# Kernel optimization log

Measured on AMD Instinct MI355X. Metric: run time of the kernel, lower is better.

## Reference

```python
import jax, jax.numpy as jnp
import numpy as np

N = 100000   # nodes
E = 1600000  # edges (avg degree 16)
D = 128      # input_dim = hidden_dim = output_dim


def setup_inputs() -> dict:
    key = jax.random.key(0)
    ks = jax.random.split(key, 16)
    s = 0.02
    inp = {
        "node_emb": jax.random.normal(ks[0], (N, D), dtype=jnp.float32),
        "edge_index": jax.random.randint(ks[1], (2, E), 0, N, dtype=jnp.int64),
        # last-layer GCN branch (conv1 -> relu -> conv2); earlier layers are dead code in SSL.forward
        "gcn_w1": jax.random.normal(ks[2], (D, D), dtype=jnp.float32) * s,
        "gcn_b1": jnp.zeros((D,), dtype=jnp.float32),
        "gcn_w2": jax.random.normal(ks[3], (D, D), dtype=jnp.float32) * s,
        "gcn_b2": jnp.zeros((D,), dtype=jnp.float32),
        # last-layer GIN branch (GINConv eps=0, Mlp == single Linear)
        "gin_w1": jax.random.normal(ks[4], (D, D), dtype=jnp.float32) * s,
        "gin_b1": jnp.zeros((D,), dtype=jnp.float32),
        "gin_w2": jax.random.normal(ks[5], (D, D), dtype=jnp.float32) * s,
        "gin_b2": jnp.zeros((D,), dtype=jnp.float32),
        # fusion heads
        "lin_w": jax.random.normal(ks[6], (D, D), dtype=jnp.float32) * s,
        "lin_b": jnp.zeros((D,), dtype=jnp.float32),
        "fc_w": jax.random.normal(ks[7], (D, D), dtype=jnp.float32) * s,
        "fc_b": jnp.zeros((D,), dtype=jnp.float32),
    }
    return inp


def reference(node_emb, edge_index, gcn_w1, gcn_b1, gcn_w2, gcn_b2,
              gin_w1, gin_b1, gin_w2, gin_b2, lin_w, lin_b, fc_w, fc_b):
    n = node_emb.shape[0]
    src, dst = edge_index[0], edge_index[1]

    # symmetric GCN normalization with self-loops: deg counts incoming edges + 1
    deg = jax.ops.segment_sum(jnp.ones(src.shape[0], node_emb.dtype), dst, num_segments=n) + 1.0
    dinv = jax.lax.rsqrt(deg)                  # deg >= 1 always
    edge_norm = dinv[src] * dinv[dst]          # [E]
    self_norm = dinv * dinv                    # [N] self-loop coefficient

    def gcn_conv(x, W, b):
        y = x @ W                                                        # [N, D]
        agg = jax.ops.segment_sum(y[src] * edge_norm[:, None], dst, num_segments=n)
        return agg + self_norm[:, None] * y + b

    def gin_conv(x, W, b):
        # GINConv(train_eps=False): nn((1+0)*x + sum_{j in N(i)} x_j), nn = Linear
        agg = jax.ops.segment_sum(x[src], dst, num_segments=n)
        return (x + agg) @ W + b

    # GCN branch: conv1 -> relu -> (dropout=identity in eval) -> conv2
    h = jax.nn.relu(gcn_conv(node_emb, gcn_w1, gcn_b1))
    x_gcn = gcn_conv(h, gcn_w2, gcn_b2)

    # GIN branch: conv1 -> conv2
    g = gin_conv(node_emb, gin_w1, gin_b1)
    x_gin = gin_conv(g, gin_w2, gin_b2)

    # fusion heads
    x_gin = x_gin @ lin_w + lin_b
    x_gcn = x_gcn @ lin_w + lin_b
    return (x_gin + x_gcn) @ fc_w + fc_b
```

## Files before the change

kernel.cpp:

```cpp
#include <hip/hip_runtime.h>

#define D 128
#define HS_LD 136

using s8v = __attribute__((ext_vector_type(8))) short;
using f4v = __attribute__((ext_vector_type(4))) float;

__device__ __forceinline__ float bf2f(ushort u) {
  union { uint i; float f; } v; v.i = ((uint)u) << 16; return v.f;
}
__device__ __forceinline__ ushort f2bf(float f) {
  union { float f; uint i; } v; v.f = f;
  uint b = v.i;
  return (ushort)((b + 0x7fffu + ((b >> 16) & 1u)) >> 16);
}

__global__ void megaA_kernel(const int* __restrict__ dst, int* __restrict__ ideg,
                             int* __restrict__ pos, int E,
                             const float* __restrict__ x, ushort* __restrict__ xb, long total,
                             const float* __restrict__ lw, const float* __restrict__ fw,
                             float* __restrict__ LF,
                             const float* __restrict__ gw1, ushort* __restrict__ T1g) {
  int b = blockIdx.x;
  if (b < 2048) {
    int i = b * 256 + threadIdx.x;
    int stride = 2048 * 256;
    for (int e = i; e < E; e += stride)
      pos[e] = atomicAdd(&ideg[dst[e]], 1);
  } else if (b < 5248) {
    long i = ((long)(b - 2048) * 256 + threadIdx.x) * 8;
    long stride = (long)3200 * 256 * 8;
    for (long t = i; t < total; t += stride) {
      float4 v0 = *(const float4*)(x + t);
      float4 v1 = *(const float4*)(x + t + 4);
      s8v u;
      u[0] = (short)f2bf(v0.x); u[1] = (short)f2bf(v0.y);
      u[2] = (short)f2bf(v0.z); u[3] = (short)f2bf(v0.w);
      u[4] = (short)f2bf(v1.x); u[5] = (short)f2bf(v1.y);
      u[6] = (short)f2bf(v1.z); u[7] = (short)f2bf(v1.w);
      *(s8v*)(xb + t) = u;
    }
  } else if (b < 5312) {
    int t = (b - 5248) * 256 + threadIdx.x;
    int r = t >> 7, c = t & 127;
    float s = 0.f;
#pragma unroll 8
    for (int k = 0; k < 128; ++k) s = fmaf(lw[r * 128 + k], fw[k * 128 + c], s);
    LF[r * 128 + c] = s;
  } else {
    int t = (b - 5312) * 256 + threadIdx.x;
    int k = t >> 7, c = t & 127;
    T1g[c * 128 + k] = f2bf(gw1[k * 128 + c]);
  }
}

__global__ void scanP_kernel(const int* __restrict__ deg, int* __restrict__ incl,
                             int* __restrict__ bsum, int n, int nb,
                             const float* __restrict__ iw2, const float* __restrict__ gw2,
                             const float* __restrict__ LF,
                             float* __restrict__ M2i, ushort* __restrict__ W2gT,
                             const float* __restrict__ gb2, const float* __restrict__ ib2,
                             const float* __restrict__ lb, const float* __restrict__ fw,
                             const float* __restrict__ fb, float* __restrict__ btot) {
  int b = blockIdx.x;
  if (b < nb) {
    __shared__ int tmp[256];
    int t = threadIdx.x;
    int i = b * 256 + t;
    int v = (i < n) ? deg[i] : 0;
    tmp[t] = v;
    __syncthreads();
#pragma unroll
    for (int off = 1; off < 256; off <<= 1) {
      int u = (t >= off) ? tmp[t - off] : 0;
      __syncthreads();
      tmp[t] += u;
      __syncthreads();
    }
    if (i < n) incl[i] = tmp[t];
    if (t == 255) bsum[b] = tmp[255];
  } else if (b < nb + 64) {
    int t = (b - nb) * 256 + threadIdx.x;
    int k = t >> 7, c = t & 127;
    float s = 0.f;
#pragma unroll 8
    for (int j = 0; j < 128; ++j) s = fmaf(iw2[k * 128 + j], LF[j * 128 + c], s);
    M2i[k * 128 + c] = s;
  } else if (b < nb + 128) {
    int t = (b - nb - 64) * 256 + threadIdx.x;
    int k = t >> 7, c = t & 127;
    float s = 0.f;
#pragma unroll 8
    for (int j = 0; j < 128; ++j) s = fmaf(gw2[k * 128 + j], LF[j * 128 + c], s);
    W2gT[c * 128 + k] = f2bf(s);
  } else if (threadIdx.x < 128) {
    int c = threadIdx.x;
    float s = fb[c];
#pragma unroll 8
    for (int j = 0; j < 128; ++j) {
      s = fmaf(gb2[j] + ib2[j], LF[j * 128 + c], s);
      s = fmaf(2.f * lb[j], fw[j * 128 + c], s);
    }
    btot[c] = s;
  }
}

__global__ void scan2F_kernel(int* __restrict__ bsum, int nb,
                              const float* __restrict__ iw1, const float* __restrict__ M2i,
                              ushort* __restrict__ WginT,
                              const float* __restrict__ ib1, float* __restrict__ bgin) {
  int b = blockIdx.x;
  if (b == 0) {
    __shared__ int tmp[256];
    __shared__ int carry_s;
    int t = threadIdx.x;
    if (t == 0) carry_s = 0;
    __syncthreads();
    for (int base = 0; base < nb; base += 256) {
      int v = (base + t < nb) ? bsum[base + t] : 0;
      tmp[t] = v;
      __syncthreads();
#pragma unroll
      for (int off = 1; off < 256; off <<= 1) {
        int u = (t >= off) ? tmp[t - off] : 0;
        __syncthreads();
        tmp[t] += u;
        __syncthreads();
      }
      int inc = tmp[t] + carry_s;
      if (base + t < nb) bsum[base + t] = inc;
      __syncthreads();
      if (t == 255) carry_s = inc;
      __syncthreads();
    }
  } else if (b <= 64) {
    int t = (b - 1) * 256 + threadIdx.x;
    int k = t >> 7, c = t & 127;
    float s = 0.f;
#pragma unroll 8
    for (int j = 0; j < 128; ++j) s = fmaf(iw1[k * 128 + j], M2i[j * 128 + c], s);
    WginT[c * 128 + k] = f2bf(s);
  } else if (threadIdx.x < 128) {
    int c = threadIdx.x;
    float s = 0.f;
#pragma unroll 8
    for (int j = 0; j < 128; ++j) s = fmaf(ib1[j], M2i[j * 128 + c], s);
    bgin[c] = s;
  }
}

__global__ void scan3_kernel(const int* __restrict__ deg, const int* __restrict__ incl,
                             const int* __restrict__ bsum, int* __restrict__ rowptr,
                             float* __restrict__ dinv, int n, int E) {
  int i = blockIdx.x * 256 + threadIdx.x;
  if (i < n) {
    int carry = (blockIdx.x > 0) ? bsum[blockIdx.x - 1] : 0;
    int d = deg[i];
    rowptr[i] = incl[i] - d + carry;
    dinv[i] = rsqrtf((float)d + 1.0f);
  }
  if (i == 0) rowptr[n] = E;
}

__global__ void scatter_kernel(const int* __restrict__ src, const int* __restrict__ dst,
                               const int* __restrict__ rowptr, const int* __restrict__ pos,
                               int* __restrict__ csrc, int E) {
  int i = blockIdx.x * blockDim.x + threadIdx.x;
  int stride = gridDim.x * blockDim.x;
  for (int e = i; e < E; e += stride)
    csrc[rowptr[dst[e]] + pos[e]] = src[e];
}

__global__ __launch_bounds__(256) void gatherA_kernel(
    const ushort* __restrict__ xb, const float* __restrict__ dinv,
    const int* __restrict__ rowptr, const int* __restrict__ csrc,
    ushort* __restrict__ ab, int n) {
  int nd = blockIdx.x * 4 + (threadIdx.x >> 6);
  if (nd >= n) return;
  int lane = threadIdx.x & 63;
  int half = lane >> 5;
  int hl = lane & 31;
  int beg = rowptr[nd], end = rowptr[nd + 1];
  float4 sg = make_float4(0.f, 0.f, 0.f, 0.f);
  float4 sc = make_float4(0.f, 0.f, 0.f, 0.f);
  int j = beg + half;
  for (; j + 6 < end; j += 8) {
    int s0 = csrc[j], s1 = csrc[j + 2], s2 = csrc[j + 4], s3 = csrc[j + 6];
    float w0 = dinv[s0], w1 = dinv[s1], w2 = dinv[s2], w3 = dinv[s3];
    ushort4 v0 = *(const ushort4*)(xb + (long)s0 * D + 4 * hl);
    ushort4 v1 = *(const ushort4*)(xb + (long)s1 * D + 4 * hl);
    ushort4 v2 = *(const ushort4*)(xb + (long)s2 * D + 4 * hl);
    ushort4 v3 = *(const ushort4*)(xb + (long)s3 * D + 4 * hl);
    float a0 = bf2f(v0.x), a1 = bf2f(v0.y), a2 = bf2f(v0.z), a3 = bf2f(v0.w);
    sg.x += a0; sg.y += a1; sg.z += a2; sg.w += a3;
    sc.x = fmaf(w0, a0, sc.x); sc.y = fmaf(w0, a1, sc.y);
    sc.z = fmaf(w0, a2, sc.z); sc.w = fmaf(w0, a3, sc.w);
    a0 = bf2f(v1.x); a1 = bf2f(v1.y); a2 = bf2f(v1.z); a3 = bf2f(v1.w);
    sg.x += a0; sg.y += a1; sg.z += a2; sg.w += a3;
    sc.x = fmaf(w1, a0, sc.x); sc.y = fmaf(w1, a1, sc.y);
    sc.z = fmaf(w1, a2, sc.z); sc.w = fmaf(w1, a3, sc.w);
    a0 = bf2f(v2.x); a1 = bf2f(v2.y); a2 = bf2f(v2.z); a3 = bf2f(v2.w);
    sg.x += a0; sg.y += a1; sg.z += a2; sg.w += a3;
    sc.x = fmaf(w2, a0, sc.x); sc.y = fmaf(w2, a1, sc.y);
    sc.z = fmaf(w2, a2, sc.z); sc.w = fmaf(w2, a3, sc.w);
    a0 = bf2f(v3.x); a1 = bf2f(v3.y); a2 = bf2f(v3.z); a3 = bf2f(v3.w);
    sg.x += a0; sg.y += a1; sg.z += a2; sg.w += a3;
    sc.x = fmaf(w3, a0, sc.x); sc.y = fmaf(w3, a1, sc.y);
    sc.z = fmaf(w3, a2, sc.z); sc.w = fmaf(w3, a3, sc.w);
  }
  for (; j < end; j += 2) {
    int s0 = csrc[j];
    float w0 = dinv[s0];
    ushort4 v0 = *(const ushort4*)(xb + (long)s0 * D + 4 * hl);
    float a0 = bf2f(v0.x), a1 = bf2f(v0.y), a2 = bf2f(v0.z), a3 = bf2f(v0.w);
    sg.x += a0; sg.y += a1; sg.z += a2; sg.w += a3;
    sc.x = fmaf(w0, a0, sc.x); sc.y = fmaf(w0, a1, sc.y);
    sc.z = fmaf(w0, a2, sc.z); sc.w = fmaf(w0, a3, sc.w);
  }
  sg.x += __shfl_xor(sg.x, 32); sg.y += __shfl_xor(sg.y, 32);
  sg.z += __shfl_xor(sg.z, 32); sg.w += __shfl_xor(sg.w, 32);
  sc.x += __shfl_xor(sc.x, 32); sc.y += __shfl_xor(sc.y, 32);
  sc.z += __shfl_xor(sc.z, 32); sc.w += __shfl_xor(sc.w, 32);

  ushort4 us = *(const ushort4*)(xb + (long)nd * D + 4 * hl);
  float x0 = bf2f(us.x), x1 = bf2f(us.y), x2 = bf2f(us.z), x3 = bf2f(us.w);
  float dd = dinv[nd];
  ushort4 o;
  if (half == 0) {
    o.x = f2bf(dd * (sc.x + dd * x0));
    o.y = f2bf(dd * (sc.y + dd * x1));
    o.z = f2bf(dd * (sc.z + dd * x2));
    o.w = f2bf(dd * (sc.w + dd * x3));
    *(ushort4*)(ab + (long)nd * 256 + 4 * hl) = o;
  } else {
    o.x = f2bf(x0 + sg.x);
    o.y = f2bf(x1 + sg.y);
    o.z = f2bf(x2 + sg.z);
    o.w = f2bf(x3 + sg.w);
    *(ushort4*)(ab + (long)nd * 256 + 128 + 4 * hl) = o;
  }
}

__global__ __launch_bounds__(256) void gemm1_kernel(
    const ushort* __restrict__ ab,
    const ushort* __restrict__ T1g, const ushort* __restrict__ WginT,
    const ushort* __restrict__ W2gT,
    const float* __restrict__ gb1, const float* __restrict__ bgin,
    ushort* __restrict__ pq, int n) {
  __shared__ ushort Ws[128 * 128];
  __shared__ ushort Hs[128 * HS_LD];
  const int y = blockIdx.y;
  const int tid = threadIdx.x;
  const int wave = tid >> 6, lane = tid & 63;
  const int rlo = lane & 15, khi = lane >> 4;
  const int rb = blockIdx.x * 128 + wave * 32;

  s8v a[2][4];
#pragma unroll
  for (int rt = 0; rt < 2; ++rt) {
    int row = rb + rt * 16 + rlo;
    row = row < n ? row : n - 1;
    const ushort* p = ab + (long)row * 256 + y * 128 + khi * 8;
#pragma unroll
    for (int ks = 0; ks < 4; ++ks) a[rt][ks] = *(const s8v*)(p + ks * 32);
  }

  {
    const ushort* W = y ? WginT : T1g;
#pragma unroll
    for (int j = 0; j < 8; ++j) {
      int q = tid + 256 * j;
      int c = q >> 4, kc = q & 15;
      *(s8v*)&Ws[c * 128 + ((kc ^ (c & 7)) << 3)] = *(const s8v*)(W + c * 128 + kc * 8);
    }
  }
  __syncthreads();

  f4v acc[2][8];
#pragma unroll
  for (int rt = 0; rt < 2; ++rt)
#pragma unroll
    for (int ct = 0; ct < 8; ++ct) acc[rt][ct] = (f4v){0.f, 0.f, 0.f, 0.f};

#pragma unroll
  for (int ks = 0; ks < 4; ++ks) {
#pragma unroll
    for (int ct = 0; ct < 8; ++ct) {
      int c = ct * 16 + rlo;
      int kc = ks * 4 + khi;
      s8v b = *(const s8v*)&Ws[c * 128 + ((kc ^ (c & 7)) << 3)];
      acc[0][ct] = __builtin_amdgcn_mfma_f32_16x16x32_bf16(a[0][ks], b, acc[0][ct], 0, 0, 0);
      acc[1][ct] = __builtin_amdgcn_mfma_f32_16x16x32_bf16(a[1][ks], b, acc[1][ct], 0, 0, 0);
    }
  }

  if (y == 1) {
#pragma unroll
    for (int ct = 0; ct < 8; ++ct) {
      int col = ct * 16 + rlo;
      float bb = bgin[col];
#pragma unroll
      for (int rt = 0; rt < 2; ++rt) {
#pragma unroll
        for (int i = 0; i < 4; ++i) {
          int row = rb + rt * 16 + 4 * khi + i;
          if (row < n)
            pq[(long)row * 256 + 128 + col] = f2bf(acc[rt][ct][i] + bb);
        }
      }
    }
    return;
  }

  __syncthreads();
#pragma unroll
  for (int ct = 0; ct < 8; ++ct) {
    int col = ct * 16 + rlo;
    float bb = gb1[col];
#pragma unroll
    for (int rt = 0; rt < 2; ++rt) {
#pragma unroll
      for (int i = 0; i < 4; ++i) {
        int r = wave * 32 + rt * 16 + 4 * khi + i;
        Hs[r * HS_LD + col] = f2bf(fmaxf(acc[rt][ct][i] + bb, 0.f));
      }
    }
  }
#pragma unroll
  for (int j = 0; j < 8; ++j) {
    int q = tid + 256 * j;
    int c = q >> 4, kc = q & 15;
    *(s8v*)&Ws[c * 128 + ((kc ^ (c & 7)) << 3)] = *(const s8v*)(W2gT + c * 128 + kc * 8);
  }
  __syncthreads();

  s8v a2[2][4];
#pragma unroll
  for (int rt = 0; rt < 2; ++rt) {
    int r = wave * 32 + rt * 16 + rlo;
#pragma unroll
    for (int ks = 0; ks < 4; ++ks)
      a2[rt][ks] = *(const s8v*)&Hs[r * HS_LD + (ks * 4 + khi) * 8];
  }

  f4v acc2[2][8];
#pragma unroll
  for (int rt = 0; rt < 2; ++rt)
#pragma unroll
    for (int ct = 0; ct < 8; ++ct) acc2[rt][ct] = (f4v){0.f, 0.f, 0.f, 0.f};

#pragma unroll
  for (int ks = 0; ks < 4; ++ks) {
#pragma unroll
    for (int ct = 0; ct < 8; ++ct) {
      int c = ct * 16 + rlo;
      int kc = ks * 4 + khi;
      s8v b = *(const s8v*)&Ws[c * 128 + ((kc ^ (c & 7)) << 3)];
      acc2[0][ct] = __builtin_amdgcn_mfma_f32_16x16x32_bf16(a2[0][ks], b, acc2[0][ct], 0, 0, 0);
      acc2[1][ct] = __builtin_amdgcn_mfma_f32_16x16x32_bf16(a2[1][ks], b, acc2[1][ct], 0, 0, 0);
    }
  }

#pragma unroll
  for (int ct = 0; ct < 8; ++ct) {
    int col = ct * 16 + rlo;
#pragma unroll
    for (int rt = 0; rt < 2; ++rt) {
#pragma unroll
      for (int i = 0; i < 4; ++i) {
        int row = rb + rt * 16 + 4 * khi + i;
        if (row < n)
          pq[(long)row * 256 + col] = f2bf(acc2[rt][ct][i]);
      }
    }
  }
}

__global__ __launch_bounds__(256) void gatherB_kernel(
    const ushort* __restrict__ pq, const float* __restrict__ dinv,
    const int* __restrict__ rowptr, const int* __restrict__ csrc,
    const float* __restrict__ btot, float* __restrict__ out, int n) {
  int nd = blockIdx.x * 4 + (threadIdx.x >> 6);
  if (nd >= n) return;
  int lane = threadIdx.x & 63;
  int half = lane >> 5;
  int hl = lane & 31;
  int beg = rowptr[nd], end = rowptr[nd + 1];
  float4 s = make_float4(0.f, 0.f, 0.f, 0.f);
  int j = beg;
  for (; j + 3 < end; j += 4) {
    int s0 = csrc[j], s1 = csrc[j + 1], s2 = csrc[j + 2], s3 = csrc[j + 3];
    float w0 = dinv[s0], w1 = dinv[s1], w2 = dinv[s2], w3 = dinv[s3];
    ushort4 v0 = *(const ushort4*)(pq + (long)s0 * 256 + lane * 4);
    ushort4 v1 = *(const ushort4*)(pq + (long)s1 * 256 + lane * 4);
    ushort4 v2 = *(const ushort4*)(pq + (long)s2 * 256 + lane * 4);
    ushort4 v3 = *(const ushort4*)(pq + (long)s3 * 256 + lane * 4);
    float c0 = half ? 1.f : w0;
    float c1 = half ? 1.f : w1;
    float c2 = half ? 1.f : w2;
    float c3 = half ? 1.f : w3;
    s.x = fmaf(c0, bf2f(v0.x), s.x); s.y = fmaf(c0, bf2f(v0.y), s.y);
    s.z = fmaf(c0, bf2f(v0.z), s.z); s.w = fmaf(c0, bf2f(v0.w), s.w);
    s.x = fmaf(c1, bf2f(v1.x), s.x); s.y = fmaf(c1, bf2f(v1.y), s.y);
    s.z = fmaf(c1, bf2f(v1.z), s.z); s.w = fmaf(c1, bf2f(v1.w), s.w);
    s.x = fmaf(c2, bf2f(v2.x), s.x); s.y = fmaf(c2, bf2f(v2.y), s.y);
    s.z = fmaf(c2, bf2f(v2.z), s.z); s.w = fmaf(c2, bf2f(v2.w), s.w);
    s.x = fmaf(c3, bf2f(v3.x), s.x); s.y = fmaf(c3, bf2f(v3.y), s.y);
    s.z = fmaf(c3, bf2f(v3.z), s.z); s.w = fmaf(c3, bf2f(v3.w), s.w);
  }
  for (; j < end; ++j) {
    int s0 = csrc[j];
    float w0 = dinv[s0];
    ushort4 v0 = *(const ushort4*)(pq + (long)s0 * 256 + lane * 4);
    float c0 = half ? 1.f : w0;
    s.x = fmaf(c0, bf2f(v0.x), s.x); s.y = fmaf(c0, bf2f(v0.y), s.y);
    s.z = fmaf(c0, bf2f(v0.z), s.z); s.w = fmaf(c0, bf2f(v0.w), s.w);
  }
  ushort4 u = *(const ushort4*)(pq + (long)nd * 256 + lane * 4);
  float dd = dinv[nd];
  float4 o;
  if (half == 0) {
    o.x = dd * (s.x + dd * bf2f(u.x));
    o.y = dd * (s.y + dd * bf2f(u.y));
    o.z = dd * (s.z + dd * bf2f(u.z));
    o.w = dd * (s.w + dd * bf2f(u.w));
  } else {
    o.x = s.x + bf2f(u.x);
    o.y = s.y + bf2f(u.y);
    o.z = s.z + bf2f(u.z);
    o.w = s.w + bf2f(u.w);
  }
  o.x += __shfl_xor(o.x, 32);
  o.y += __shfl_xor(o.y, 32);
  o.z += __shfl_xor(o.z, 32);
  o.w += __shfl_xor(o.w, 32);
  if (half == 0) {
    float4 bt = *(const float4*)(btot + 4 * hl);
    o.x += bt.x; o.y += bt.y; o.z += bt.z; o.w += bt.w;
    *(float4*)(out + (long)nd * D + 4 * hl) = o;
  }
}

extern "C" void kernel_launch(void* const* d_in, const int* in_sizes, int n_in,
                              void* d_out, int out_size, void* d_ws, size_t ws_size,
                              hipStream_t stream) {
  const float* x   = (const float*)d_in[0];
  const int*   ei  = (const int*)d_in[1];
  const float* gw1 = (const float*)d_in[2];
  const float* gb1 = (const float*)d_in[3];
  const float* gw2 = (const float*)d_in[4];
  const float* gb2 = (const float*)d_in[5];
  const float* iw1 = (const float*)d_in[6];
  const float* ib1 = (const float*)d_in[7];
  const float* iw2 = (const float*)d_in[8];
  const float* ib2 = (const float*)d_in[9];
  const float* lw  = (const float*)d_in[10];
  const float* lb  = (const float*)d_in[11];
  const float* fw  = (const float*)d_in[12];
  const float* fb  = (const float*)d_in[13];
  float* out = (float*)d_out;

  const int n = in_sizes[0] / D;
  const int E = in_sizes[1] / 2;
  const int* src = ei;
  const int* dst = ei + E;
  const int nb = (n + 255) / 256;
  const long ND = (long)n * D;

  char* p = (char*)d_ws;
  auto alloc = [&](size_t bytes) {
    char* r = p;
    p += (bytes + 255) & ~(size_t)255;
    return r;
  };
  int* ideg    = (int*)alloc((size_t)n * 4);
  int* incl    = (int*)alloc((size_t)n * 4);
  int* rowptr  = (int*)alloc((size_t)(n + 1) * 4);
  int* bsum    = (int*)alloc(1024 * 4);
  int* pos     = (int*)alloc((size_t)E * 4);
  int* csrc    = (int*)alloc((size_t)E * 4);
  float* dinv  = (float*)alloc((size_t)n * 4);
  float* LF    = (float*)alloc(16384 * 4);
  float* M2i   = (float*)alloc(16384 * 4);
  float* btot  = (float*)alloc(128 * 4);
  float* bgin  = (float*)alloc(128 * 4);
  ushort* xb   = (ushort*)alloc(ND * 2);
  ushort* T1g   = (ushort*)alloc(16384 * 2);
  ushort* WginT = (ushort*)alloc(16384 * 2);
  ushort* W2gT  = (ushort*)alloc(16384 * 2);
  ushort* ab   = (ushort*)alloc(2 * ND * 2);
  ushort* pq   = (ushort*)alloc(2 * ND * 2);

  hipMemsetAsync(ideg, 0, (size_t)n * 4, stream);

  megaA_kernel<<<5376, 256, 0, stream>>>(dst, ideg, pos, E, x, xb, ND, lw, fw, LF, gw1, T1g);
  scanP_kernel<<<nb + 129, 256, 0, stream>>>(ideg, incl, bsum, n, nb, iw2, gw2, LF,
                                             M2i, W2gT, gb2, ib2, lb, fw, fb, btot);
  scan2F_kernel<<<66, 256, 0, stream>>>(bsum, nb, iw1, M2i, WginT, ib1, bgin);
  scan3_kernel<<<nb, 256, 0, stream>>>(ideg, incl, bsum, rowptr, dinv, n, E);
  scatter_kernel<<<2048, 256, 0, stream>>>(src, dst, rowptr, pos, csrc, E);

  gatherA_kernel<<<(n + 3) / 4, 256, 0, stream>>>(xb, dinv, rowptr, csrc, ab, n);
  const int nblk = (n + 127) / 128;
  gemm1_kernel<<<dim3(nblk, 2), 256, 0, stream>>>(ab, T1g, WginT, W2gT, gb1, bgin, pq, n);
  gatherB_kernel<<<(n + 3) / 4, 256, 0, stream>>>(pq, dinv, rowptr, csrc, btot, out, n);
}
```

Before: 374.3 us.

## Pack source index with dinv in CSR and prescale GCN rows by dinv

The scatter kernel now writes an int2 per CSR edge holding the source id and that source's dinv. gatherA reads the weight from this contiguous array instead of doing a random dinv lookup per edge. gemm1 multiplies its output rows by dinv before writing pq, so gatherB sums neighbour rows without any per-edge weight and drops its dinv gathers and FMAs. In exchange, the CSR array doubles in size and the scatter kernel does one extra random dinv read per edge. Correctness depends on the prescale being applied only to the GCN half of pq.

```diff
diff --git a/kernel.cpp b/kernel.cpp
--- a/kernel.cpp
+++ b/kernel.cpp
@@ -164,16 +164,19 @@
 
 __global__ void scatter_kernel(const int* __restrict__ src, const int* __restrict__ dst,
                                const int* __restrict__ rowptr, const int* __restrict__ pos,
-                               int* __restrict__ csrc, int E) {
+                               const float* __restrict__ dinv,
+                               int2* __restrict__ cdata, int E) {
   int i = blockIdx.x * blockDim.x + threadIdx.x;
   int stride = gridDim.x * blockDim.x;
-  for (int e = i; e < E; e += stride)
-    csrc[rowptr[dst[e]] + pos[e]] = src[e];
+  for (int e = i; e < E; e += stride) {
+    int s = src[e];
+    cdata[rowptr[dst[e]] + pos[e]] = make_int2(s, __float_as_int(dinv[s]));
+  }
 }
 
 __global__ __launch_bounds__(256) void gatherA_kernel(
     const ushort* __restrict__ xb, const float* __restrict__ dinv,
-    const int* __restrict__ rowptr, const int* __restrict__ csrc,
+    const int* __restrict__ rowptr, const int2* __restrict__ cd,
     ushort* __restrict__ ab, int n) {
   int nd = blockIdx.x * 4 + (threadIdx.x >> 6);
   if (nd >= n) return;
@@ -185,12 +188,13 @@
   float4 sc = make_float4(0.f, 0.f, 0.f, 0.f);
   int j = beg + half;
   for (; j + 6 < end; j += 8) {
-    int s0 = csrc[j], s1 = csrc[j + 2], s2 = csrc[j + 4], s3 = csrc[j + 6];
-    float w0 = dinv[s0], w1 = dinv[s1], w2 = dinv[s2], w3 = dinv[s3];
-    ushort4 v0 = *(const ushort4*)(xb + (long)s0 * D + 4 * hl);
-    ushort4 v1 = *(const ushort4*)(xb + (long)s1 * D + 4 * hl);
-    ushort4 v2 = *(const ushort4*)(xb + (long)s2 * D + 4 * hl);
-    ushort4 v3 = *(const ushort4*)(xb + (long)s3 * D + 4 * hl);
+    int2 c0 = cd[j], c1 = cd[j + 2], c2 = cd[j + 4], c3 = cd[j + 6];
+    float w0 = __int_as_float(c0.y), w1 = __int_as_float(c1.y);
+    float w2 = __int_as_float(c2.y), w3 = __int_as_float(c3.y);
+    ushort4 v0 = *(const ushort4*)(xb + (long)c0.x * D + 4 * hl);
+    ushort4 v1 = *(const ushort4*)(xb + (long)c1.x * D + 4 * hl);
+    ushort4 v2 = *(const ushort4*)(xb + (long)c2.x * D + 4 * hl);
+    ushort4 v3 = *(const ushort4*)(xb + (long)c3.x * D + 4 * hl);
     float a0 = bf2f(v0.x), a1 = bf2f(v0.y), a2 = bf2f(v0.z), a3 = bf2f(v0.w);
     sg.x += a0; sg.y += a1; sg.z += a2; sg.w += a3;
     sc.x = fmaf(w0, a0, sc.x); sc.y = fmaf(w0, a1, sc.y);
@@ -209,9 +213,9 @@
     sc.z = fmaf(w3, a2, sc.z); sc.w = fmaf(w3, a3, sc.w);
   }
   for (; j < end; j += 2) {
-    int s0 = csrc[j];
-    float w0 = dinv[s0];
-    ushort4 v0 = *(const ushort4*)(xb + (long)s0 * D + 4 * hl);
+    int2 c0 = cd[j];
+    float w0 = __int_as_float(c0.y);
+    ushort4 v0 = *(const ushort4*)(xb + (long)c0.x * D + 4 * hl);
     float a0 = bf2f(v0.x), a1 = bf2f(v0.y), a2 = bf2f(v0.z), a3 = bf2f(v0.w);
     sg.x += a0; sg.y += a1; sg.z += a2; sg.w += a3;
     sc.x = fmaf(w0, a0, sc.x); sc.y = fmaf(w0, a1, sc.y);
@@ -246,6 +250,7 @@
     const ushort* __restrict__ T1g, const ushort* __restrict__ WginT,
     const ushort* __restrict__ W2gT,
     const float* __restrict__ gb1, const float* __restrict__ bgin,
+    const float* __restrict__ dinv,
     ushort* __restrict__ pq, int n) {
   __shared__ ushort Ws[128 * 128];
   __shared__ ushort Hs[128 * HS_LD];
@@ -361,6 +366,15 @@
     }
   }
 
+  float ddv[2][4];
+#pragma unroll
+  for (int rt = 0; rt < 2; ++rt)
+#pragma unroll
+    for (int i = 0; i < 4; ++i) {
+      int row = rb + rt * 16 + 4 * khi + i;
+      ddv[rt][i] = (row < n) ? dinv[row] : 0.f;
+    }
+
 #pragma unroll
   for (int ct = 0; ct < 8; ++ct) {
     int col = ct * 16 + rlo;
@@ -370,7 +384,7 @@
       for (int i = 0; i < 4; ++i) {
         int row = rb + rt * 16 + 4 * khi + i;
         if (row < n)
-          pq[(long)row * 256 + col] = f2bf(acc2[rt][ct][i]);
+          pq[(long)row * 256 + col] = f2bf(ddv[rt][i] * acc2[rt][ct][i]);
       }
     }
   }
@@ -378,7 +392,7 @@
 
 __global__ __launch_bounds__(256) void gatherB_kernel(
     const ushort* __restrict__ pq, const float* __restrict__ dinv,
-    const int* __restrict__ rowptr, const int* __restrict__ csrc,
+    const int* __restrict__ rowptr, const int2* __restrict__ cd,
     const float* __restrict__ btot, float* __restrict__ out, int n) {
   int nd = blockIdx.x * 4 + (threadIdx.x >> 6);
   if (nd >= n) return;
@@ -389,41 +403,30 @@
   float4 s = make_float4(0.f, 0.f, 0.f, 0.f);
   int j = beg;
   for (; j + 3 < end; j += 4) {
-    int s0 = csrc[j], s1 = csrc[j + 1], s2 = csrc[j + 2], s3 = csrc[j + 3];
-    float w0 = dinv[s0], w1 = dinv[s1], w2 = dinv[s2], w3 = dinv[s3];
+    int s0 = cd[j].x, s1 = cd[j + 1].x, s2 = cd[j + 2].x, s3 = cd[j + 3].x;
     ushort4 v0 = *(const ushort4*)(pq + (long)s0 * 256 + lane * 4);
     ushort4 v1 = *(const ushort4*)(pq + (long)s1 * 256 + lane * 4);
     ushort4 v2 = *(const ushort4*)(pq + (long)s2 * 256 + lane * 4);
     ushort4 v3 = *(const ushort4*)(pq + (long)s3 * 256 + lane * 4);
-    float c0 = half ? 1.f : w0;
-    float c1 = half ? 1.f : w1;
-    float c2 = half ? 1.f : w2;
-    float c3 = half ? 1.f : w3;
-    s.x = fmaf(c0, bf2f(v0.x), s.x); s.y = fmaf(c0, bf2f(v0.y), s.y);
-    s.z = fmaf(c0, bf2f(v0.z), s.z); s.w = fmaf(c0, bf2f(v0.w), s.w);
-    s.x = fmaf(c1, bf2f(v1.x), s.x); s.y = fmaf(c1, bf2f(v1.y), s.y);
-    s.z = fmaf(c1, bf2f(v1.z), s.z); s.w = fmaf(c1, bf2f(v1.w), s.w);
-    s.x = fmaf(c2, bf2f(v2.x), s.x); s.y = fmaf(c2, bf2f(v2.y), s.y);
-    s.z = fmaf(c2, bf2f(v2.z), s.z); s.w = fmaf(c2, bf2f(v2.w), s.w);
-    s.x = fmaf(c3, bf2f(v3.x), s.x); s.y = fmaf(c3, bf2f(v3.y), s.y);
-    s.z = fmaf(c3, bf2f(v3.z), s.z); s.w = fmaf(c3, bf2f(v3.w), s.w);
+    s.x += (bf2f(v0.x) + bf2f(v1.x)) + (bf2f(v2.x) + bf2f(v3.x));
+    s.y += (bf2f(v0.y) + bf2f(v1.y)) + (bf2f(v2.y) + bf2f(v3.y));
+    s.z += (bf2f(v0.z) + bf2f(v1.z)) + (bf2f(v2.z) + bf2f(v3.z));
+    s.w += (bf2f(v0.w) + bf2f(v1.w)) + (bf2f(v2.w) + bf2f(v3.w));
   }
   for (; j < end; ++j) {
-    int s0 = csrc[j];
-    float w0 = dinv[s0];
+    int s0 = cd[j].x;
     ushort4 v0 = *(const ushort4*)(pq + (long)s0 * 256 + lane * 4);
-    float c0 = half ? 1.f : w0;
-    s.x = fmaf(c0, bf2f(v0.x), s.x); s.y = fmaf(c0, bf2f(v0.y), s.y);
-    s.z = fmaf(c0, bf2f(v0.z), s.z); s.w = fmaf(c0, bf2f(v0.w), s.w);
+    s.x += bf2f(v0.x); s.y += bf2f(v0.y);
+    s.z += bf2f(v0.z); s.w += bf2f(v0.w);
   }
   ushort4 u = *(const ushort4*)(pq + (long)nd * 256 + lane * 4);
   float dd = dinv[nd];
   float4 o;
   if (half == 0) {
-    o.x = dd * (s.x + dd * bf2f(u.x));
-    o.y = dd * (s.y + dd * bf2f(u.y));
-    o.z = dd * (s.z + dd * bf2f(u.z));
-    o.w = dd * (s.w + dd * bf2f(u.w));
+    o.x = dd * (s.x + bf2f(u.x));
+    o.y = dd * (s.y + bf2f(u.y));
+    o.z = dd * (s.z + bf2f(u.z));
+    o.w = dd * (s.w + bf2f(u.w));
   } else {
     o.x = s.x + bf2f(u.x);
     o.y = s.y + bf2f(u.y);
@@ -478,7 +481,7 @@
   int* rowptr  = (int*)alloc((size_t)(n + 1) * 4);
   int* bsum    = (int*)alloc(1024 * 4);
   int* pos     = (int*)alloc((size_t)E * 4);
-  int* csrc    = (int*)alloc((size_t)E * 4);
+  int2* cdata  = (int2*)alloc((size_t)E * 8);
   float* dinv  = (float*)alloc((size_t)n * 4);
   float* LF    = (float*)alloc(16384 * 4);
   float* M2i   = (float*)alloc(16384 * 4);
@@ -498,10 +501,10 @@
                                              M2i, W2gT, gb2, ib2, lb, fw, fb, btot);
   scan2F_kernel<<<66, 256, 0, stream>>>(bsum, nb, iw1, M2i, WginT, ib1, bgin);
   scan3_kernel<<<nb, 256, 0, stream>>>(ideg, incl, bsum, rowptr, dinv, n, E);
-  scatter_kernel<<<2048, 256, 0, stream>>>(src, dst, rowptr, pos, csrc, E);
-
-  gatherA_kernel<<<(n + 3) / 4, 256, 0, stream>>>(xb, dinv, rowptr, csrc, ab, n);
+  scatter_kernel<<<2048, 256, 0, stream>>>(src, dst, rowptr, pos, dinv, cdata, E);
+
+  gatherA_kernel<<<(n + 3) / 4, 256, 0, stream>>>(xb, dinv, rowptr, cdata, ab, n);
   const int nblk = (n + 127) / 128;
-  gemm1_kernel<<<dim3(nblk, 2), 256, 0, stream>>>(ab, T1g, WginT, W2gT, gb1, bgin, pq, n);
-  gatherB_kernel<<<(n + 3) / 4, 256, 0, stream>>>(pq, dinv, rowptr, csrc, btot, out, n);
-}
+  gemm1_kernel<<<dim3(nblk, 2), 256, 0, stream>>>(ab, T1g, WginT, W2gT, gb1, bgin, dinv, pq, n);
+  gatherB_kernel<<<(n + 3) / 4, 256, 0, stream>>>(pq, dinv, rowptr, cdata, btot, out, n);
+}
```

Result: slower. 394.1 us (+5.3%).
